# Performance work log

Hardware: AMD Instinct MI355X
Metric: run time of the kernel (lower is better)

The kernel has to match this reference:

```python
import jax, jax.numpy as jnp
import numpy as np

K_KDE = 64
K_RIPS = 16
SCALE = 20.0
DESTNUM = 5
SQRT2 = 1.4142135623730951


def _knn(x, k):
    # squared-euclidean kNN (self included), mirrors FAISS IndexFlatL2 search
    sq = jnp.sum(x * x, axis=1)
    d2 = jnp.maximum(sq[:, None] + sq[None, :] - 2.0 * (x @ x.T), 0.0)
    neg_d, idx = jax.lax.top_k(-d2, k)
    return -neg_d, idx


def _density_map(x, k, scale):
    # KDE density: sum of RBF kernels over k nearest neighbours, max-normalized
    d2, idx = _knn(x, k)
    dens = jnp.sum(jnp.exp(-d2 / scale), axis=1) / (k * scale)
    return dens / jnp.max(dens), idx


def _cluster_pairs(density_sorted, rips_idxs):
    # ToMATo-style union-find over points in decreasing density order.
    # density_sorted is ascending, so index == density rank (inherently
    # sequential on host, as in the original torch module).
    N = density_sorted.shape[0]
    root = np.arange(N)

    def find(i):
        while root[i] != i:
            root[i] = root[root[i]]
            i = root[i]
        return i

    pairs = []
    for i in range(N - 2, -1, -1):
        us = rips_idxs[i][rips_idxs[i] > i]  # upper star: higher-density nbrs
        if us.size == 0:
            continue  # local maximum: births a new cluster
        root[i] = find(int(us.max()))
        for j in us:
            rj, ri = find(int(j)), find(i)
            if rj != ri:
                lo, hi = (ri, rj) if ri < rj else (rj, ri)
                if density_sorted[lo] - density_sorted[i] < 1.0:  # threshold=1
                    root[lo] = hi
                    pairs.append((lo, i))
    see = np.array(pairs, dtype=np.int64)
    # per birth peak, keep the earliest (highest-density) death index
    pd = []
    for b in np.unique(see[:, 0]):
        pd.append([b, see[see[:, 0] == b, 1].max()])
    return np.array(pd, dtype=np.int64)


def setup_inputs() -> dict:
    key = jax.random.key(0)
    x = jax.random.normal(key, (4096, 16), dtype=jnp.float32)
    return {"x": x}


def reference(x):
    kde_dists, kde_idxs = _density_map(x, K_KDE, SCALE)
    sorted_idxs = jnp.argsort(kde_dists)                 # ascending density
    kde_dists_s = kde_dists[sorted_idxs]
    inv_perm = jnp.argsort(sorted_idxs)                  # inverse permutation
    kde_idxs_s = inv_perm[kde_idxs[sorted_idxs]]         # newI1 remap
    pc = x[sorted_idxs]
    _, rips_idxs = _knn(pc, K_RIPS)                      # Rips graph on sorted pc
    pd_pairs = jnp.asarray(
        _cluster_pairs(
            np.asarray(jax.device_get(kde_dists_s)),
            np.asarray(jax.device_get(rips_idxs)),
        )
    )  # [M, 2] (birth_idx, death_idx)
    oripd = kde_dists_s[pd_pairs]                        # [M, 2] densities
    order = jnp.argsort(oripd[:, 0] - oripd[:, 1])       # by persistence, asc
    changepairs = pd_pairs[order[:-DESTNUM]]             # pairs to kill
    nochangepairs = pd_pairs[order[-DESTNUM:-1]]         # pairs to keep
    dest = oripd[order[-1]]                              # most persistent pair
    pd11 = kde_dists_s[changepairs]
    weakdist = jnp.sum(pd11[:, 0] - pd11[:, 1]) / SQRT2
    strongdist = jnp.sum(jnp.linalg.norm(kde_dists_s[nochangepairs] - dest, axis=1))
    return weakdist + strongdist, rips_idxs
```

## Files before the change

### kernel.cpp

```cpp
#include <hip/hip_runtime.h>

#define NPTS 4096
#define DIM 16
#define KKDE 64
#define KRIPS 16
#define CANDCAP 512

typedef unsigned long long u64;
typedef unsigned int u32;
typedef unsigned short u16;

__device__ inline float xla_expf_fma(float input) {
  float x = fminf(input, 88.3762626647950f);
  x = fmaxf(x, -88.3762626647949f);
  float fx = floorf(__builtin_fmaf(x, 1.44269504088896341f, 0.5f));
  x = __builtin_fmaf(fx, -0.693359375f, x);
  x = __builtin_fmaf(fx, 2.12194440e-4f, x);
  float z = __fmul_rn(x, x);
  float y = __builtin_fmaf(x, 1.9875691500e-4f, 1.3981999507e-3f);
  y = __builtin_fmaf(y, x, 8.3334519073e-3f);
  y = __builtin_fmaf(y, x, 4.1665795894e-2f);
  y = __builtin_fmaf(y, x, 1.6666665459e-1f);
  y = __builtin_fmaf(y, x, 5.0000001201e-1f);
  y = __builtin_fmaf(y, z, x);
  y = __fadd_rn(1.0f, y);
  int n = (int)fx;
  float p2n = __uint_as_float(((u32)(n + 127)) << 23);
  return fmaxf(__fmul_rn(y, p2n), input);
}

__device__ inline float llvm_tree16(const float* a) {
  float b[8], c[4], d[2];
#pragma unroll
  for (int j = 0; j < 8; j++) b[j] = __fadd_rn(a[j], a[j + 8]);
#pragma unroll
  for (int j = 0; j < 4; j++) c[j] = __fadd_rn(b[j], b[j + 4]);
  d[0] = __fadd_rn(c[0], c[2]);
  d[1] = __fadd_rn(c[1], c[3]);
  return __fadd_rn(d[0], d[1]);
}

__device__ inline float sq16(const float* v) {
  float p[16];
#pragma unroll
  for (int d = 0; d < 16; d++) p[d] = __fmul_rn(v[d], v[d]);
  return llvm_tree16(p);
}

__device__ inline float d2_formula(float sqi, float sqj, float acc) {
  float d2 = __builtin_fmaf(-2.0f, acc, __fadd_rn(sqi, sqj));
  return fmaxf(d2, 0.0f);
}

__global__ __launch_bounds__(256) void dens_kernel(const float* __restrict__ x,
                                                   float* __restrict__ dens,
                                                   u16* __restrict__ knnj) {
  __shared__ u32 hist[4096];
  __shared__ u32 csum[256];
  __shared__ u64 cand[CANDCAP];
  __shared__ float e_sh[KKDE];
  __shared__ float xish[DIM];
  __shared__ int sh_chunkB, sh_baseChunk, sh_B, sh_cnt;
  const int i = blockIdx.x;
  const int tid = threadIdx.x;
  for (int h = tid; h < 4096; h += 256) hist[h] = 0u;
  if (tid < DIM) xish[tid] = x[i * DIM + tid];
  if (tid == 0) sh_cnt = 0;
  __syncthreads();
  float xi[16];
#pragma unroll
  for (int d = 0; d < 16; d++) xi[d] = xish[d];
  const float sqi = sq16(xi);
  u64 keys[16];
#pragma unroll
  for (int s = 0; s < NPTS / 256; s++) {
    int j = tid + 256 * s;
    const float4* xp = (const float4*)(x + j * DIM);
    float4 b0 = xp[0], b1 = xp[1], b2 = xp[2], b3 = xp[3];
    float xj[16] = {b0.x, b0.y, b0.z, b0.w, b1.x, b1.y, b1.z, b1.w,
                    b2.x, b2.y, b2.z, b2.w, b3.x, b3.y, b3.z, b3.w};
    float acc = 0.f;
#pragma unroll
    for (int d = 0; d < 16; d++) acc = __builtin_fmaf(xi[d], xj[d], acc);
    float d2 = d2_formula(sqi, sq16(xj), acc);
    u64 key = (((u64)__float_as_uint(d2)) << 32) | (u32)j;
    keys[s] = key;
    atomicAdd(&hist[(u32)(key >> 52)], 1u);
  }
  __syncthreads();
  u32 cs = 0;
#pragma unroll
  for (int b2 = 0; b2 < 16; b2++) cs += hist[tid * 16 + b2];
  csum[tid] = cs;
  __syncthreads();
  for (int off = 1; off < 256; off <<= 1) {
    u32 v = csum[tid];
    u32 add = (tid >= off) ? csum[tid - off] : 0u;
    __syncthreads();
    csum[tid] = v + add;
    __syncthreads();
  }
  if (csum[tid] >= KKDE && (tid == 0 || csum[tid - 1] < KKDE)) {
    sh_chunkB = tid;
    sh_baseChunk = (tid == 0) ? 0 : (int)csum[tid - 1];
  }
  __syncthreads();
  if (tid < 16) {
    int h = (int)hist[sh_chunkB * 16 + tid];
    int cum = h;
#pragma unroll
    for (int off = 1; off < 16; off <<= 1) {
      int o = __shfl_up(cum, off, 16);
      if (tid >= off) cum += o;
    }
    int prev = cum - h;
    if (sh_baseChunk + cum >= KKDE && sh_baseChunk + prev < KKDE)
      sh_B = sh_chunkB * 16 + tid;
  }
  __syncthreads();
  const u32 B = (u32)sh_B;
#pragma unroll
  for (int s = 0; s < NPTS / 256; s++) {
    if ((u32)(keys[s] >> 52) <= B) {
      int pos = atomicAdd(&sh_cnt, 1);
      if (pos < CANDCAP) cand[pos] = keys[s];
    }
  }
  __syncthreads();
  const int cnt = (sh_cnt < CANDCAP) ? sh_cnt : CANDCAP;
  for (int c = tid; c < cnt; c += 256) {
    u64 mykey = cand[c];
    int rank = 0;
    for (int t = 0; t < cnt; t++) rank += (cand[t] < mykey) ? 1 : 0;
    if (rank < KKDE) {
      knnj[i * KKDE + rank] = (u16)(mykey & 0xFFFFull);
      float d2v = __uint_as_float((u32)(mykey >> 32));
      e_sh[rank] = xla_expf_fma(__fmul_rn(-d2v, 0.05f));
    }
  }
  __syncthreads();
  if (tid == 0) {
    float lane[16];
#pragma unroll
    for (int j = 0; j < 16; j++) lane[j] = e_sh[j];
#pragma unroll
    for (int k = 1; k < 4; k++)
#pragma unroll
      for (int j = 0; j < 16; j++)
        lane[j] = __fadd_rn(lane[j], e_sh[16 * k + j]);
    float s = llvm_tree16(lane);
    dens[i] = __fmul_rn(s, (1.0f / 1280.0f));
  }
}

__device__ inline void bitonicM(u64* k, int tid, int M) {
  for (int ksz = 2; ksz <= M; ksz <<= 1) {
    for (int jsz = ksz >> 1; jsz > 0; jsz >>= 1) {
      __syncthreads();
      for (int idx = tid; idx < M; idx += 1024) {
        int ixj = idx ^ jsz;
        if (ixj > idx) {
          bool up = ((idx & ksz) == 0);
          u64 a = k[idx], b = k[ixj];
          if ((a > b) == up) { k[idx] = b; k[ixj] = a; }
        }
      }
    }
  }
  __syncthreads();
}

__global__ __launch_bounds__(1024) void sort_kernel(const float* __restrict__ dens,
                                                    int* __restrict__ sidx,
                                                    float* __restrict__ dens_s,
                                                    int* __restrict__ invp) {
  __shared__ u64 k[NPTS];
  __shared__ float red[1024];
  int tid = threadIdx.x;
  float m = 0.0f;
  for (int i = tid; i < NPTS; i += 1024) m = fmaxf(m, dens[i]);
  red[tid] = m;
  __syncthreads();
  for (int off = 512; off > 0; off >>= 1) {
    if (tid < off) red[tid] = fmaxf(red[tid], red[tid + off]);
    __syncthreads();
  }
  float mx = red[0];
  for (int i = tid; i < NPTS; i += 1024) {
    float dn = __fdiv_rn(dens[i], mx);
    k[i] = (((u64)__float_as_uint(dn)) << 32) | (u32)i;
  }
  bitonicM(k, tid, NPTS);
  for (int i = tid; i < NPTS; i += 1024) {
    u64 key = k[i];
    int si = (int)(key & 0xffffffffull);
    sidx[i] = si;
    invp[si] = i;
    dens_s[i] = __uint_as_float((u32)(key >> 32));
  }
}

__global__ __launch_bounds__(64) void rips_kernel(const float* __restrict__ x,
                                                  const int* __restrict__ sidx,
                                                  const int* __restrict__ invp,
                                                  const u16* __restrict__ knnj,
                                                  u16* __restrict__ rips,
                                                  int* __restrict__ maxu,
                                                  float* __restrict__ outIdx) {
  const int p = blockIdx.x;
  const int lane = threadIdx.x;
  const int s0 = sidx[p];
  float xi[16];
  const float4* xip = (const float4*)(x + s0 * DIM);
  float4 i0 = xip[0], i1 = xip[1], i2 = xip[2], i3 = xip[3];
  xi[0] = i0.x; xi[1] = i0.y; xi[2] = i0.z; xi[3] = i0.w;
  xi[4] = i1.x; xi[5] = i1.y; xi[6] = i1.z; xi[7] = i1.w;
  xi[8] = i2.x; xi[9] = i2.y; xi[10] = i2.z; xi[11] = i2.w;
  xi[12] = i3.x; xi[13] = i3.y; xi[14] = i3.z; xi[15] = i3.w;
  const float sqi = sq16(xi);
  int j = (int)knnj[s0 * KKDE + lane];
  const float4* xp = (const float4*)(x + j * DIM);
  float4 b0 = xp[0], b1 = xp[1], b2 = xp[2], b3 = xp[3];
  float xj[16] = {b0.x, b0.y, b0.z, b0.w, b1.x, b1.y, b1.z, b1.w,
                  b2.x, b2.y, b2.z, b2.w, b3.x, b3.y, b3.z, b3.w};
  float acc = 0.f;
#pragma unroll
  for (int d = 0; d < 16; d++) acc = __builtin_fmaf(xi[d], xj[d], acc);
  float d2 = d2_formula(sqi, sq16(xj), acc);
  int q = invp[j];
  u64 key = (((u64)__float_as_uint(d2)) << 32) | (u32)q;
#pragma unroll
  for (int ksz = 2; ksz <= 64; ksz <<= 1) {
#pragma unroll
    for (int jm = 32; jm > 0; jm >>= 1) {
      if (jm < ksz) {
        u64 partner = __shfl_xor(key, jm);
        bool up = ((lane & ksz) == 0);
        bool low = ((lane & jm) == 0);
        u64 mn = (partner < key) ? partner : key;
        u64 mx = (partner < key) ? key : partner;
        key = (low == up) ? mn : mx;
      }
    }
  }
  int wj = (int)(key & 0xffffffffull);
  if (lane < KRIPS) {
    rips[p * KRIPS + lane] = (u16)wj;
    outIdx[p * KRIPS + lane] = (float)wj;
  }
  int mu = (lane < KRIPS && wj > p) ? wj : -1;
#pragma unroll
  for (int off = 32; off > 0; off >>= 1) {
    int o = __shfl_xor(mu, off);
    mu = (o > mu) ? o : mu;
  }
  if (lane == 0) maxu[p] = mu;
}

__device__ inline int uf_find(int* root, int v) {
  while (true) {
    int p = root[v];
    if (p == v) return v;
    int g = root[p];
    if (g == p) return p;
    root[v] = g;
    v = g;
  }
}

__global__ __launch_bounds__(1024) void uf_kernel(const u16* __restrict__ rips,
                                                  const int* __restrict__ maxu,
                                                  int* __restrict__ pairs,
                                                  const float* __restrict__ dens_s,
                                                  float* __restrict__ out0) {
  __shared__ __align__(16) char smem0[NPTS * 8];
  int* root = (int*)smem0;
  int* death = (int*)(smem0 + NPTS * 4);
  u64* kk = (u64*)smem0;
  __shared__ u32 jr[4096];
  __shared__ int elist[256];
  __shared__ u32 mask[8];
  __shared__ int scanb[1024];
  __shared__ double red[1024];
  const int tid = threadIdx.x;
  const int slot = tid & 15;
  for (int v = tid; v < NPTS; v += 1024) {
    int m = maxu[v];
    root[v] = (m >= 0) ? m : v;
    death[v] = -1;
  }
  if (tid < 8) mask[tid] = 0u;
  __syncthreads();
  for (int it = 0; it < 13; it++) {
    for (int v = tid; v < NPTS; v += 1024) root[v] = root[root[v]];
    __syncthreads();
  }
  for (int b = (NPTS / 256) - 1; b >= 0; b--) {
#pragma unroll
    for (int p = 0; p < 4; p++) {
      int ii_local = p * 64 + (tid >> 4);
      int ii = b * 256 + ii_local;
      int jj = -1;
      if (ii <= NPTS - 2) {
        int t = (int)rips[ii * KRIPS + slot];
        if (t > ii) jj = t;
      }
      int r = (jj >= 0) ? uf_find(root, jj) : -1;
      jr[ii_local * 16 + slot] = (jj >= 0) ? (u32)r : ~0u;
      const int wg = (tid & 63) >> 4;
      u64 vb = __ballot(jj >= 0);
      u32 vs = (u32)((vb >> (wg * 16)) & 0xFFFFull);
      int fl = wg * 16 + (vs ? (__ffs(vs) - 1) : 0);
      int fv = __shfl(r, fl);
      u64 db = __ballot(jj >= 0 && r != fv);
      bool flagged = (vs != 0u) && (((db >> (wg * 16)) & 0xFFFFull) != 0ull);
      if (slot == 0 && flagged)
        atomicOr(&mask[ii_local >> 5], 1u << (ii_local & 31));
    }
    __syncthreads();
    if (tid < 64) {
      const int lane = tid;
      const int g = lane >> 4;
      const int sl = lane & 15;
      int ne = 0;
      {
        int cnt = 0;
#pragma unroll
        for (int w = 7; w >= 0; w--) cnt += __popc(mask[w]);
        ne = cnt;
      }
      for (int base2 = 0; base2 < ne; base2 += 64) {
        int k2 = base2 + lane;
        if (k2 < ne) {
          int cnt = 0, ev2 = -1;
#pragma unroll
          for (int w = 7; w >= 0; w--) {
            u32 mwv = mask[w];
            int c = __popc(mwv);
            if (ev2 < 0 && k2 < cnt + c) {
              int need = k2 - cnt;
              u32 m = mwv;
              for (int t2 = 0; t2 < need; t2++) m &= ~(1u << (31 - __clz(m)));
              ev2 = w * 32 + (31 - __clz(m));
            }
            cnt += c;
          }
          elist[k2] = ev2;
        }
      }
      asm volatile("s_waitcnt lgkmcnt(0)" ::: "memory");
      int e_nx = (g < ne) ? elist[g] : -1;
      u32 jrw_nx = (e_nx >= 0) ? jr[e_nx * 16 + sl] : ~0u;
      for (int k4 = 0; k4 < ne; k4 += 4) {
        const int e = e_nx;
        const u32 jrw = jrw_nx;
        {
          int idx2 = k4 + 4 + g;
          e_nx = (idx2 < ne) ? elist[idx2] : -1;
          jrw_nx = (e_nx >= 0) ? jr[e_nx * 16 + sl] : ~0u;
        }
        const bool act = (jrw != ~0u);
        int rr0 = act ? (int)jrw : 0;
        int pv = root[rr0];
        int rr = -1;
        if (act) rr = (pv == rr0) ? rr0 : uf_find(root, rr0);
        int t = act ? rr : -1;
#pragma unroll
        for (int off = 8; off > 0; off >>= 1) {
          int o = __shfl_xor(t, off, 16);
          t = (o > t) ? o : t;
        }
        int mx = t;
        const int ev = (e >= 0) ? (b * 256 + e) : -1;
#pragma unroll
        for (int gg = 0; gg < 4; gg++) {
          u64 kb = __ballot(act && rr != mx);
          u32 kg = (u32)((kb >> (gg * 16)) & 0xFFFFull);
          while (kg) {
            int tl = gg * 16 + (__ffs(kg) - 1);
            kg &= kg - 1;
            int kr = __shfl(rr, tl);
            int mxg = __shfl(mx, tl);
            if (kr != mxg) {
              int ig = __shfl(ev, tl);
              if (lane == 0) { root[kr] = mxg; death[kr] = ig; }
              bool hit = act && (rr == kr);
              u64 hb = __ballot(hit);
              if (hit) rr = mxg;
              if ((hb >> (g * 16)) & 0xFFFFull) mx = (mxg > mx) ? mxg : mx;
            }
          }
        }
      }
      if (lane < 8) mask[lane] = 0u;
    }
    __syncthreads();
  }
  int base = tid * 4;
  int l0 = death[base + 0], l1 = death[base + 1];
  int l2 = death[base + 2], l3 = death[base + 3];
  int c = (l0 >= 0) + (l1 >= 0) + (l2 >= 0) + (l3 >= 0);
  scanb[tid] = c;
  __syncthreads();
  for (int off = 1; off < 1024; off <<= 1) {
    int add = (tid >= off) ? scanb[tid - off] : 0;
    __syncthreads();
    scanb[tid] += add;
    __syncthreads();
  }
  int pos = scanb[tid] - c;
  if (l0 >= 0) { pairs[2 * pos] = base + 0; pairs[2 * pos + 1] = l0; pos++; }
  if (l1 >= 0) { pairs[2 * pos] = base + 1; pairs[2 * pos + 1] = l1; pos++; }
  if (l2 >= 0) { pairs[2 * pos] = base + 2; pairs[2 * pos + 1] = l2; pos++; }
  if (l3 >= 0) { pairs[2 * pos] = base + 3; pairs[2 * pos + 1] = l3; pos++; }
  const int P = scanb[1023];
  __syncthreads();
  int M = 256;
  while (M < P) M <<= 1;
  for (int i = tid; i < M; i += 1024) {
    u64 key = ~0ull;
    if (i < P) {
      float pe = __fsub_rn(dens_s[pairs[2 * i]], dens_s[pairs[2 * i + 1]]);
      key = (((u64)__float_as_uint(pe)) << 32) | (u32)i;
    }
    kk[i] = key;
  }
  bitonicM(kk, tid, M);
  double a = 0.0;
  const int lim = P - 5;
  for (int rnk = tid; rnk < lim; rnk += 1024) {
    int pp = (int)(kk[rnk] & 0xffffffffull);
    a += (double)(dens_s[pairs[2 * pp]] - dens_s[pairs[2 * pp + 1]]);
  }
  red[tid] = a;
  __syncthreads();
  for (int off = 512; off > 0; off >>= 1) {
    if (tid < off) red[tid] += red[tid + off];
    __syncthreads();
  }
  if (tid == 0 && P > 0) {
    double weakdist = red[0] / 1.4142135623730951;
    int plast = (int)(kk[P - 1] & 0xffffffffull);
    float dest0 = dens_s[pairs[2 * plast]];
    float dest1 = dens_s[pairs[2 * plast + 1]];
    double strong = 0.0;
    for (int rnk = P - 5; rnk <= P - 2; rnk++) {
      if (rnk < 0) continue;
      int pp = (int)(kk[rnk] & 0xffffffffull);
      double dx = (double)dens_s[pairs[2 * pp]] - (double)dest0;
      double dy = (double)dens_s[pairs[2 * pp + 1]] - (double)dest1;
      strong += sqrt(dx * dx + dy * dy);
    }
    out0[0] = (float)(weakdist + strong);
  }
}

extern "C" void kernel_launch(void* const* d_in, const int* in_sizes, int n_in,
                              void* d_out, int out_size, void* d_ws, size_t ws_size,
                              hipStream_t stream) {
  const float* x = (const float*)d_in[0];
  float* out = (float*)d_out;
  char* ws = (char*)d_ws;
  size_t off = 0;
  float* dens = (float*)(ws + off);   off += NPTS * 4;
  float* dens_s = (float*)(ws + off); off += NPTS * 4;
  int* sidx = (int*)(ws + off);       off += NPTS * 4;
  int* invp = (int*)(ws + off);       off += NPTS * 4;
  int* maxu = (int*)(ws + off);       off += NPTS * 4;
  u16* rips = (u16*)(ws + off);       off += NPTS * KRIPS * 2;
  int* pairs = (int*)(ws + off);      off += NPTS * 2 * 4;
  u16* knnj = (u16*)(ws + off);       off += NPTS * KKDE * 2;

  dens_kernel<<<dim3(NPTS), dim3(256), 0, stream>>>(x, dens, knnj);
  sort_kernel<<<dim3(1), dim3(1024), 0, stream>>>(dens, sidx, dens_s, invp);
  rips_kernel<<<dim3(NPTS), dim3(64), 0, stream>>>(x, sidx, invp, knnj,
                                                   rips, maxu, out + 1);
  uf_kernel<<<dim3(1), dim3(1024), 0, stream>>>(rips, maxu, pairs, dens_s, out);
}
```

Measured before the change: 266.8 us.

## Process two query points per density block and register-resident bitonic sort

The density kernel now handles two query points per block, so each loaded neighbour row and its squared norm are reused for two distance computations and the launch uses half as many blocks. Selection per query still runs sequentially with its own histogram and candidate buffers, which doubles shared memory use and lowers occupancy. The sort kernel keeps four keys per thread in registers. It uses in-register compare-exchange for large strides, shared memory for middle strides and wavefront shuffles for strides under 64, which cuts shared-memory traffic and barriers.

```diff
diff --git a/kernel.cpp b/kernel.cpp
--- a/kernel.cpp
+++ b/kernel.cpp
@@ -55,23 +55,25 @@
 __global__ __launch_bounds__(256) void dens_kernel(const float* __restrict__ x,
                                                    float* __restrict__ dens,
                                                    u16* __restrict__ knnj) {
-  __shared__ u32 hist[4096];
+  __shared__ u32 hist[2][4096];
   __shared__ u32 csum[256];
-  __shared__ u64 cand[CANDCAP];
+  __shared__ u64 cand[2][CANDCAP];
   __shared__ float e_sh[KKDE];
-  __shared__ float xish[DIM];
-  __shared__ int sh_chunkB, sh_baseChunk, sh_B, sh_cnt;
-  const int i = blockIdx.x;
+  __shared__ float xish[2 * DIM];
+  __shared__ int sh_chunkB, sh_baseChunk, sh_B;
+  __shared__ int sh_cnt[2];
+  const int i0 = blockIdx.x * 2;
   const int tid = threadIdx.x;
-  for (int h = tid; h < 4096; h += 256) hist[h] = 0u;
-  if (tid < DIM) xish[tid] = x[i * DIM + tid];
-  if (tid == 0) sh_cnt = 0;
-  __syncthreads();
-  float xi[16];
-#pragma unroll
-  for (int d = 0; d < 16; d++) xi[d] = xish[d];
-  const float sqi = sq16(xi);
-  u64 keys[16];
+  for (int h = tid; h < 4096; h += 256) { hist[0][h] = 0u; hist[1][h] = 0u; }
+  if (tid < 2 * DIM) xish[tid] = x[i0 * DIM + tid];
+  if (tid < 2) sh_cnt[tid] = 0;
+  __syncthreads();
+  float xi0[16], xi1[16];
+#pragma unroll
+  for (int d = 0; d < 16; d++) { xi0[d] = xish[d]; xi1[d] = xish[16 + d]; }
+  const float sqi0 = sq16(xi0);
+  const float sqi1 = sq16(xi1);
+  u64 keys0[16], keys1[16];
 #pragma unroll
   for (int s = 0; s < NPTS / 256; s++) {
     int j = tid + 256 * s;
@@ -79,77 +81,90 @@
     float4 b0 = xp[0], b1 = xp[1], b2 = xp[2], b3 = xp[3];
     float xj[16] = {b0.x, b0.y, b0.z, b0.w, b1.x, b1.y, b1.z, b1.w,
                     b2.x, b2.y, b2.z, b2.w, b3.x, b3.y, b3.z, b3.w};
-    float acc = 0.f;
-#pragma unroll
-    for (int d = 0; d < 16; d++) acc = __builtin_fmaf(xi[d], xj[d], acc);
-    float d2 = d2_formula(sqi, sq16(xj), acc);
-    u64 key = (((u64)__float_as_uint(d2)) << 32) | (u32)j;
-    keys[s] = key;
-    atomicAdd(&hist[(u32)(key >> 52)], 1u);
-  }
-  __syncthreads();
-  u32 cs = 0;
-#pragma unroll
-  for (int b2 = 0; b2 < 16; b2++) cs += hist[tid * 16 + b2];
-  csum[tid] = cs;
-  __syncthreads();
-  for (int off = 1; off < 256; off <<= 1) {
-    u32 v = csum[tid];
-    u32 add = (tid >= off) ? csum[tid - off] : 0u;
-    __syncthreads();
-    csum[tid] = v + add;
-    __syncthreads();
-  }
-  if (csum[tid] >= KKDE && (tid == 0 || csum[tid - 1] < KKDE)) {
-    sh_chunkB = tid;
-    sh_baseChunk = (tid == 0) ? 0 : (int)csum[tid - 1];
-  }
-  __syncthreads();
-  if (tid < 16) {
-    int h = (int)hist[sh_chunkB * 16 + tid];
-    int cum = h;
-#pragma unroll
-    for (int off = 1; off < 16; off <<= 1) {
-      int o = __shfl_up(cum, off, 16);
-      if (tid >= off) cum += o;
-    }
-    int prev = cum - h;
-    if (sh_baseChunk + cum >= KKDE && sh_baseChunk + prev < KKDE)
-      sh_B = sh_chunkB * 16 + tid;
-  }
-  __syncthreads();
-  const u32 B = (u32)sh_B;
-#pragma unroll
-  for (int s = 0; s < NPTS / 256; s++) {
-    if ((u32)(keys[s] >> 52) <= B) {
-      int pos = atomicAdd(&sh_cnt, 1);
-      if (pos < CANDCAP) cand[pos] = keys[s];
-    }
-  }
-  __syncthreads();
-  const int cnt = (sh_cnt < CANDCAP) ? sh_cnt : CANDCAP;
-  for (int c = tid; c < cnt; c += 256) {
-    u64 mykey = cand[c];
-    int rank = 0;
-    for (int t = 0; t < cnt; t++) rank += (cand[t] < mykey) ? 1 : 0;
-    if (rank < KKDE) {
-      knnj[i * KKDE + rank] = (u16)(mykey & 0xFFFFull);
-      float d2v = __uint_as_float((u32)(mykey >> 32));
-      e_sh[rank] = xla_expf_fma(__fmul_rn(-d2v, 0.05f));
-    }
-  }
-  __syncthreads();
-  if (tid == 0) {
-    float lane[16];
-#pragma unroll
-    for (int j = 0; j < 16; j++) lane[j] = e_sh[j];
-#pragma unroll
-    for (int k = 1; k < 4; k++)
-#pragma unroll
-      for (int j = 0; j < 16; j++)
-        lane[j] = __fadd_rn(lane[j], e_sh[16 * k + j]);
-    float s = llvm_tree16(lane);
-    dens[i] = __fmul_rn(s, (1.0f / 1280.0f));
+    float sqj = sq16(xj);
+    float acc0 = 0.f, acc1 = 0.f;
+#pragma unroll
+    for (int d = 0; d < 16; d++) acc0 = __builtin_fmaf(xi0[d], xj[d], acc0);
+#pragma unroll
+    for (int d = 0; d < 16; d++) acc1 = __builtin_fmaf(xi1[d], xj[d], acc1);
+    float d20 = d2_formula(sqi0, sqj, acc0);
+    float d21 = d2_formula(sqi1, sqj, acc1);
+    u64 key0 = (((u64)__float_as_uint(d20)) << 32) | (u32)j;
+    u64 key1 = (((u64)__float_as_uint(d21)) << 32) | (u32)j;
+    keys0[s] = key0;
+    keys1[s] = key1;
+    atomicAdd(&hist[0][(u32)(key0 >> 52)], 1u);
+    atomicAdd(&hist[1][(u32)(key1 >> 52)], 1u);
+  }
+  __syncthreads();
+#pragma unroll
+  for (int p = 0; p < 2; p++) {
+    const int ip = i0 + p;
+    u32 cs = 0;
+#pragma unroll
+    for (int b2 = 0; b2 < 16; b2++) cs += hist[p][tid * 16 + b2];
+    csum[tid] = cs;
+    __syncthreads();
+    for (int off = 1; off < 256; off <<= 1) {
+      u32 v = csum[tid];
+      u32 add = (tid >= off) ? csum[tid - off] : 0u;
+      __syncthreads();
+      csum[tid] = v + add;
+      __syncthreads();
+    }
+    if (csum[tid] >= KKDE && (tid == 0 || csum[tid - 1] < KKDE)) {
+      sh_chunkB = tid;
+      sh_baseChunk = (tid == 0) ? 0 : (int)csum[tid - 1];
+    }
+    __syncthreads();
+    if (tid < 16) {
+      int h = (int)hist[p][sh_chunkB * 16 + tid];
+      int cum = h;
+#pragma unroll
+      for (int off = 1; off < 16; off <<= 1) {
+        int o = __shfl_up(cum, off, 16);
+        if (tid >= off) cum += o;
+      }
+      int prev = cum - h;
+      if (sh_baseChunk + cum >= KKDE && sh_baseChunk + prev < KKDE)
+        sh_B = sh_chunkB * 16 + tid;
+    }
+    __syncthreads();
+    const u32 B = (u32)sh_B;
+#pragma unroll
+    for (int s = 0; s < NPTS / 256; s++) {
+      u64 ky = p ? keys1[s] : keys0[s];
+      if ((u32)(ky >> 52) <= B) {
+        int pos = atomicAdd(&sh_cnt[p], 1);
+        if (pos < CANDCAP) cand[p][pos] = ky;
+      }
+    }
+    __syncthreads();
+    const int cnt = (sh_cnt[p] < CANDCAP) ? sh_cnt[p] : CANDCAP;
+    for (int c = tid; c < cnt; c += 256) {
+      u64 mykey = cand[p][c];
+      int rank = 0;
+      for (int t = 0; t < cnt; t++) rank += (cand[p][t] < mykey) ? 1 : 0;
+      if (rank < KKDE) {
+        knnj[ip * KKDE + rank] = (u16)(mykey & 0xFFFFull);
+        float d2v = __uint_as_float((u32)(mykey >> 32));
+        e_sh[rank] = xla_expf_fma(__fmul_rn(-d2v, 0.05f));
+      }
+    }
+    __syncthreads();
+    if (tid == 0) {
+      float lane[16];
+#pragma unroll
+      for (int j = 0; j < 16; j++) lane[j] = e_sh[j];
+#pragma unroll
+      for (int k = 1; k < 4; k++)
+#pragma unroll
+        for (int j = 0; j < 16; j++)
+          lane[j] = __fadd_rn(lane[j], e_sh[16 * k + j]);
+      float s = llvm_tree16(lane);
+      dens[ip] = __fmul_rn(s, (1.0f / 1280.0f));
+    }
+    __syncthreads();
   }
 }
 
@@ -176,7 +191,7 @@
                                                     int* __restrict__ invp) {
   __shared__ u64 k[NPTS];
   __shared__ float red[1024];
-  int tid = threadIdx.x;
+  const int tid = threadIdx.x;
   float m = 0.0f;
   for (int i = tid; i < NPTS; i += 1024) m = fmaxf(m, dens[i]);
   red[tid] = m;
@@ -186,13 +201,64 @@
     __syncthreads();
   }
   float mx = red[0];
-  for (int i = tid; i < NPTS; i += 1024) {
+  u64 v[4];
+#pragma unroll
+  for (int p = 0; p < 4; p++) {
+    int i = p * 1024 + tid;
     float dn = __fdiv_rn(dens[i], mx);
-    k[i] = (((u64)__float_as_uint(dn)) << 32) | (u32)i;
-  }
-  bitonicM(k, tid, NPTS);
-  for (int i = tid; i < NPTS; i += 1024) {
-    u64 key = k[i];
+    v[p] = (((u64)__float_as_uint(dn)) << 32) | (u32)i;
+  }
+  for (int ksz = 2; ksz <= NPTS; ksz <<= 1) {
+    for (int jsz = ksz >> 1; jsz > 0; jsz >>= 1) {
+      if (jsz >= 1024) {
+        const int bit = jsz >> 10;
+#pragma unroll
+        for (int p = 0; p < 4; p++) {
+          if ((p & bit) == 0) {
+            int q = p | bit;
+            int idxl = p * 1024 + tid;
+            bool up = ((idxl & ksz) == 0);
+            u64 a = v[p], b = v[q];
+            u64 mn = (a < b) ? a : b, mxv = (a < b) ? b : a;
+            v[p] = up ? mn : mxv;
+            v[q] = up ? mxv : mn;
+          }
+        }
+      } else if (jsz >= 64) {
+        __syncthreads();
+#pragma unroll
+        for (int p = 0; p < 4; p++) k[p * 1024 + tid] = v[p];
+        __syncthreads();
+#pragma unroll
+        for (int p = 0; p < 4; p++) {
+          int idx = p * 1024 + tid;
+          u64 partner = k[idx ^ jsz];
+          bool low = ((tid & jsz) == 0);
+          bool up = ((idx & ksz) == 0);
+          u64 a = v[p];
+          u64 mn = (a < partner) ? a : partner;
+          u64 mxv = (a < partner) ? partner : a;
+          v[p] = (low == up) ? mn : mxv;
+        }
+      } else {
+#pragma unroll
+        for (int p = 0; p < 4; p++) {
+          int idx = p * 1024 + tid;
+          u64 partner = __shfl_xor(v[p], jsz);
+          bool low = ((tid & jsz) == 0);
+          bool up = ((idx & ksz) == 0);
+          u64 a = v[p];
+          u64 mn = (a < partner) ? a : partner;
+          u64 mxv = (a < partner) ? partner : a;
+          v[p] = (low == up) ? mn : mxv;
+        }
+      }
+    }
+  }
+#pragma unroll
+  for (int p = 0; p < 4; p++) {
+    int i = p * 1024 + tid;
+    u64 key = v[p];
     int si = (int)(key & 0xffffffffull);
     sidx[i] = si;
     invp[si] = i;
@@ -471,7 +537,7 @@
   int* pairs = (int*)(ws + off);      off += NPTS * 2 * 4;
   u16* knnj = (u16*)(ws + off);       off += NPTS * KKDE * 2;
 
-  dens_kernel<<<dim3(NPTS), dim3(256), 0, stream>>>(x, dens, knnj);
+  dens_kernel<<<dim3(NPTS / 2), dim3(256), 0, stream>>>(x, dens, knnj);
   sort_kernel<<<dim3(1), dim3(1024), 0, stream>>>(dens, sidx, dens_s, invp);
   rips_kernel<<<dim3(NPTS), dim3(64), 0, stream>>>(x, sidx, invp, knnj,
                                                    rips, maxu, out + 1);
```

Measured after the change: 244.1 us. 1.09x faster.
